# Optimization experiments

Measured on AMD Instinct MI355X. Metric: run time of the kernel, lower is better.

Reference implementation:

```python
import jax, jax.numpy as jnp
import numpy as np

ROI_POOLING_SIZE = 7
CROP = ROI_POOLING_SIZE * 2  # before_pooling_size = 14


def _crop_and_resize(img, boxes, crop):
    """tf.image.crop_and_resize (bilinear, extrapolation_value=0) for a single image.

    img:   [H, W, C]
    boxes: [N, 4] normalized [y1, x1, y2, x2]
    returns [N, crop, crop, C]
    """
    H, W, C = img.shape
    y1, x1, y2, x2 = boxes[:, 0], boxes[:, 1], boxes[:, 2], boxes[:, 3]
    idx = jnp.arange(crop, dtype=img.dtype)  # crop > 1 branch of TF semantics
    # sample coordinates in source-pixel space: [N, crop]
    ys = y1[:, None] * (H - 1) + idx[None, :] * ((y2 - y1) * (H - 1) / (crop - 1))[:, None]
    xs = x1[:, None] * (W - 1) + idx[None, :] * ((x2 - x1) * (W - 1) / (crop - 1))[:, None]

    y0f = jnp.floor(ys)
    x0f = jnp.floor(xs)
    ly = ys - y0f  # bilinear fractional weights [N, crop]
    lx = xs - x0f

    y0 = jnp.clip(y0f.astype(jnp.int32), 0, H - 1)
    y1i = jnp.clip(y0 + 1, 0, H - 1)
    x0 = jnp.clip(x0f.astype(jnp.int32), 0, W - 1)
    x1i = jnp.clip(x0 + 1, 0, W - 1)

    # out-of-image samples get extrapolation_value = 0
    vy = (ys >= 0) & (ys <= H - 1)  # [N, crop]
    vx = (xs >= 0) & (xs <= W - 1)

    # irregular per-box bilinear gather: val[n,i,j,c] = img[y[n,i], x[n,j], c]
    def g(yi, xi):
        return img[yi[:, :, None], xi[:, None, :]]  # [N, crop, crop, C]

    v00 = g(y0, x0)
    v01 = g(y0, x1i)
    v10 = g(y1i, x0)
    v11 = g(y1i, x1i)

    lxb = lx[:, None, :, None]
    lyb = ly[:, :, None, None]
    top = v00 + (v01 - v00) * lxb
    bot = v10 + (v11 - v10) * lxb
    val = top + (bot - top) * lyb

    valid = (vy[:, :, None] & vx[:, None, :])[..., None]
    return jnp.where(valid, val, jnp.zeros((), dtype=img.dtype))


def reference(feature_maps, proposals, image_shape):
    # proposals are pixel-space [x1, y1, x2, y2]; normalize to [y1/h, x1/w, y2/h, x2/w]
    h = image_shape[0].astype(jnp.float32)
    w = image_shape[1].astype(jnp.float32)
    boxes = jnp.stack(
        [proposals[:, 1] / h, proposals[:, 0] / w, proposals[:, 3] / h, proposals[:, 2] / w],
        axis=1,
    )
    crops = _crop_and_resize(feature_maps[0], boxes, CROP)  # [N, 14, 14, C]
    N, Hc, Wc, C = crops.shape
    # MaxPooling2D(pool=2, stride=2, padding='same'); 14 is even so no padding needed
    pooled = crops.reshape(N, Hc // 2, 2, Wc // 2, 2, C).max(axis=(2, 4))
    return pooled  # [N, 7, 7, C]


def setup_inputs() -> dict:
    key = jax.random.key(0)
    k1, k2, k3, k4, k5 = jax.random.split(key, 5)
    H_img, W_img = 800, 1216
    N = 2000
    feature_maps = jax.random.normal(k1, (1, 200, 304, 256), dtype=jnp.float32)
    # realistic boxes in image pixel coords [x1, y1, x2, y2]
    x1 = jax.random.uniform(k2, (N,), minval=0.0, maxval=0.75 * W_img)
    y1 = jax.random.uniform(k3, (N,), minval=0.0, maxval=0.75 * H_img)
    bw = jax.random.uniform(k4, (N,), minval=16.0, maxval=0.25 * W_img)
    bh = jax.random.uniform(k5, (N,), minval=16.0, maxval=0.25 * H_img)
    proposals = jnp.stack([x1, y1, jnp.minimum(x1 + bw, W_img - 1.0), jnp.minimum(y1 + bh, H_img - 1.0)], axis=1).astype(jnp.float32)
    image_shape = jnp.array([H_img, W_img], dtype=jnp.int32)
    return {"feature_maps": feature_maps, "proposals": proposals, "image_shape": image_shape}
```

## Files before the change

### kernel.cpp

```cpp
#include <hip/hip_runtime.h>
#include <math.h>

#define H_FM 200
#define W_FM 304
#define C_FM 256
#define NPIX (H_FM * W_FM)
#define CROP 14
#define PH 7
#define NPOS 49
#define NSAMP (NPOS * 4)
#define SLABS 16
#define SLAB_C 16
#define SLAB_ELEMS (NPIX * SLAB_C)
#define SPIXB (SLAB_C * 4)
#define PIXB (C_FM * 4)

typedef float floatx4 __attribute__((ext_vector_type(4)));

#define TP 16
__global__ __launch_bounds__(256) void repack_kernel(
    const float* __restrict__ fm,
    float*       __restrict__ slabbed)
{
    __shared__ float lds[TP][C_FM + 4];
    const int tid = threadIdx.x;
    const int p0  = blockIdx.x * TP;

    const float4* src = (const float4*)(fm + (size_t)p0 * C_FM);
    #pragma unroll
    for (int i = 0; i < 4; ++i) {
        const int idx = i * 256 + tid;
        const float4 v = src[idx];
        const int pix = idx >> 6;
        const int c4  = idx & 63;
        *(float4*)&lds[pix][c4 * 4] = v;
    }
    __syncthreads();

    const int s = tid >> 4;
    const int j = tid & 15;
    float* dst = slabbed + (size_t)s * SLAB_ELEMS + (size_t)p0 * SLAB_C;
    #pragma unroll
    for (int k = 0; k < 4; ++k) {
        const int m   = k * 16 + j;
        const int pix = m >> 2;
        const int cq  = m & 3;
        const float4 v = *(const float4*)&lds[pix][s * SLAB_C + cq * 4];
        *(float4*)(dst + m * 4) = v;
    }
}

__global__ __launch_bounds__(256) void roi_pool_slab_kernel(
    const float* __restrict__ slabbed,
    const float* __restrict__ proposals,
    const int*   __restrict__ image_shape,
    float*       __restrict__ out,
    int N)
{
    __shared__ uint2  gOD[224];
    __shared__ float4 gW[224];

    const int bid   = blockIdx.x;
    const int xcd   = bid & 7;
    const int jj    = bid >> 3;
    const int phase = jj / N;
    const int n     = jj - phase * N;
    const int slab  = phase * 8 + xcd;

    const int tid = threadIdx.x;

    if (tid < NSAMP) {
        const int s  = tid & 3;
        const int p  = tid >> 2;
        const int py = p / PH;
        const int px = p - py * PH;
        const int a  = s >> 1;
        const int b  = s & 1;

        const float himg = (float)image_shape[0];
        const float wimg = (float)image_shape[1];

        const float bx1 = proposals[n * 4 + 0] / wimg;
        const float by1 = proposals[n * 4 + 1] / himg;
        const float bx2 = proposals[n * 4 + 2] / wimg;
        const float by2 = proposals[n * 4 + 3] / himg;

        const float Hm1 = (float)(H_FM - 1);
        const float Wm1 = (float)(W_FM - 1);

        const float ystep = (by2 - by1) * Hm1 / (float)(CROP - 1);
        const float xstep = (bx2 - bx1) * Wm1 / (float)(CROP - 1);
        const float ys = by1 * Hm1 + (float)(2 * py + a) * ystep;
        const float xs = bx1 * Wm1 + (float)(2 * px + b) * xstep;

        const float y0f = floorf(ys);
        const float x0f = floorf(xs);
        const float ly  = ys - y0f;
        const float lx  = xs - x0f;

        int y0 = min(max((int)y0f, 0), H_FM - 1);
        int x0 = min(max((int)x0f, 0), W_FM - 1);
        const int dy = min(y0 + 1, H_FM - 1) - y0;
        const int dx = min(x0 + 1, W_FM - 1) - x0;

        const bool valid = (ys >= 0.0f) && (ys <= Hm1) &&
                           (xs >= 0.0f) && (xs <= Wm1);
        const float vf   = valid ? 1.0f : 0.0f;
        const float omlx = 1.0f - lx;
        const float omly = 1.0f - ly;

        float4 w;
        w.x = omlx * omly * vf;
        w.y = lx   * omly * vf;
        w.z = omlx * ly   * vf;
        w.w = lx   * ly   * vf;

        uint2 od;
        od.x = (uint32_t)(y0 * W_FM + x0) * SPIXB;
        od.y = (uint32_t)(dx * SPIXB) | ((uint32_t)(dy * W_FM * SPIXB) << 16);

        const int esk = tid + (tid >> 3);
        gOD[esk] = od;
        gW[esk]  = w;
    }
    __syncthreads();

    const int wave = tid >> 6;
    const int lane = tid & 63;
    const int p    = wave * 16 + (lane >> 2);
    const int q    = lane & 3;
    const int pa   = min(p, NPOS - 1);

    const char* base = (const char*)slabbed + (size_t)slab * (SLAB_ELEMS * sizeof(float));
    const uint32_t qB = (uint32_t)q * 16u;

    float4 m;
    #pragma unroll
    for (int s = 0; s < 4; ++s) {
        const int e   = pa * 4 + s;
        const int esk = e + (e >> 3);
        const uint2  od = gOD[esk];
        const float4 w  = gW[esk];

        const uint32_t o00 = od.x + qB;
        const uint32_t dxB = od.y & 0xffffu;
        const uint32_t dyB = od.y >> 16;

        const float4 t00 = *(const float4*)(base + o00);
        const float4 t01 = *(const float4*)(base + o00 + dxB);
        const float4 t10 = *(const float4*)(base + o00 + dyB);
        const float4 t11 = *(const float4*)(base + o00 + dxB + dyB);

        float4 v;
        v.x = fmaf(t00.x, w.x, fmaf(t01.x, w.y, fmaf(t10.x, w.z, t11.x * w.w)));
        v.y = fmaf(t00.y, w.x, fmaf(t01.y, w.y, fmaf(t10.y, w.z, t11.y * w.w)));
        v.z = fmaf(t00.z, w.x, fmaf(t01.z, w.y, fmaf(t10.z, w.z, t11.z * w.w)));
        v.w = fmaf(t00.w, w.x, fmaf(t01.w, w.y, fmaf(t10.w, w.z, t11.w * w.w)));

        if (s == 0) {
            m = v;
        } else {
            m.x = fmaxf(m.x, v.x);
            m.y = fmaxf(m.y, v.y);
            m.z = fmaxf(m.z, v.z);
            m.w = fmaxf(m.w, v.w);
        }
    }

    if (p < NPOS) {
        floatx4 mv;
        mv.x = m.x; mv.y = m.y; mv.z = m.z; mv.w = m.w;
        __builtin_nontemporal_store(mv,
            (floatx4*)(out + ((size_t)n * NPOS + p) * C_FM + slab * SLAB_C + q * 4));
    }
}

__global__ __launch_bounds__(256) void roi_pool_direct_kernel(
    const float* __restrict__ fm,
    const float* __restrict__ proposals,
    const int*   __restrict__ image_shape,
    float*       __restrict__ out,
    int N)
{
    __shared__ uint4  gO[NSAMP];
    __shared__ float4 gWf[NSAMP];

    const int n   = blockIdx.x;
    const int tid = threadIdx.x;

    if (tid < NSAMP) {
        const int s  = tid & 3;
        const int p  = tid >> 2;
        const int py = p / PH;
        const int px = p - py * PH;
        const int a  = s >> 1;
        const int b  = s & 1;

        const float himg = (float)image_shape[0];
        const float wimg = (float)image_shape[1];
        const float bx1 = proposals[n * 4 + 0] / wimg;
        const float by1 = proposals[n * 4 + 1] / himg;
        const float bx2 = proposals[n * 4 + 2] / wimg;
        const float by2 = proposals[n * 4 + 3] / himg;

        const float Hm1 = (float)(H_FM - 1);
        const float Wm1 = (float)(W_FM - 1);
        const float ystep = (by2 - by1) * Hm1 / (float)(CROP - 1);
        const float xstep = (bx2 - bx1) * Wm1 / (float)(CROP - 1);
        const float ys = by1 * Hm1 + (float)(2 * py + a) * ystep;
        const float xs = bx1 * Wm1 + (float)(2 * px + b) * xstep;

        const float y0f = floorf(ys);
        const float x0f = floorf(xs);
        const float ly  = ys - y0f;
        const float lx  = xs - x0f;
        int y0 = min(max((int)y0f, 0), H_FM - 1);
        int x0 = min(max((int)x0f, 0), W_FM - 1);
        const int dy = min(y0 + 1, H_FM - 1) - y0;
        const int dx = min(x0 + 1, W_FM - 1) - x0;
        const bool valid = (ys >= 0.0f) && (ys <= Hm1) &&
                           (xs >= 0.0f) && (xs <= Wm1);
        const float vf   = valid ? 1.0f : 0.0f;
        const float omlx = 1.0f - lx;
        const float omly = 1.0f - ly;

        float4 w;
        w.x = omlx * omly * vf;
        w.y = lx   * omly * vf;
        w.z = omlx * ly   * vf;
        w.w = lx   * ly   * vf;

        uint4 o;
        o.x = (uint32_t)(y0 * W_FM + x0) * PIXB;
        o.y = (uint32_t)dx * PIXB;
        o.z = (uint32_t)(dy * W_FM) * PIXB;
        o.w = 0u;
        gO[tid]  = o;
        gWf[tid] = w;
    }
    __syncthreads();

    const int wave = tid >> 6;
    const int lane = tid & 63;
    const uint32_t laneB = (uint32_t)lane * 16u;
    const char* fmB  = (const char*)fm;
    char*       outB = (char*)out + (size_t)n * (NPOS * PIXB);

    const int pbeg = (wave * NPOS) >> 2;
    const int pend = ((wave + 1) * NPOS) >> 2;

    for (int p = pbeg; p < pend; ++p) {
        float4 m;
        #pragma unroll
        for (int s = 0; s < 4; ++s) {
            const uint4  o = gO[p * 4 + s];
            const float4 w = gWf[p * 4 + s];
            const uint32_t o00 = o.x + laneB;
            const float4 t00 = *(const float4*)(fmB + o00);
            const float4 t01 = *(const float4*)(fmB + o00 + o.y);
            const float4 t10 = *(const float4*)(fmB + o00 + o.z);
            const float4 t11 = *(const float4*)(fmB + o00 + o.y + o.z);
            float4 v;
            v.x = fmaf(t00.x, w.x, fmaf(t01.x, w.y, fmaf(t10.x, w.z, t11.x * w.w)));
            v.y = fmaf(t00.y, w.x, fmaf(t01.y, w.y, fmaf(t10.y, w.z, t11.y * w.w)));
            v.z = fmaf(t00.z, w.x, fmaf(t01.z, w.y, fmaf(t10.z, w.z, t11.z * w.w)));
            v.w = fmaf(t00.w, w.x, fmaf(t01.w, w.y, fmaf(t10.w, w.z, t11.w * w.w)));
            if (s == 0) { m = v; }
            else {
                m.x = fmaxf(m.x, v.x); m.y = fmaxf(m.y, v.y);
                m.z = fmaxf(m.z, v.z); m.w = fmaxf(m.w, v.w);
            }
        }
        floatx4 mv;
        mv.x = m.x; mv.y = m.y; mv.z = m.z; mv.w = m.w;
        __builtin_nontemporal_store(mv,
            (floatx4*)(outB + (uint32_t)p * PIXB + laneB));
    }
}

extern "C" void kernel_launch(void* const* d_in, const int* in_sizes, int n_in,
                              void* d_out, int out_size, void* d_ws, size_t ws_size,
                              hipStream_t stream) {
    (void)n_in; (void)out_size;

    const float* fm        = (const float*)d_in[0];
    const float* proposals = (const float*)d_in[1];
    const int*   imshape   = (const int*)d_in[2];
    float* out = (float*)d_out;

    const int N = in_sizes[1] / 4;
    const size_t needed = (size_t)SLABS * SLAB_ELEMS * sizeof(float);

    if (ws_size >= needed) {
        repack_kernel<<<NPIX / TP, 256, 0, stream>>>(fm, (float*)d_ws);
        roi_pool_slab_kernel<<<SLABS * N, 256, 0, stream>>>(
            (const float*)d_ws, proposals, imshape, out, N);
    } else {
        roi_pool_direct_kernel<<<N, 256, 0, stream>>>(
            fm, proposals, imshape, out, N);
    }
}
```

Before: 215.5 us.

## Precompute ROI sample geometry in separate kernel and batch gathers in pool kernel

Adds a geom_kernel that computes per-sample offsets and bilinear weights for all ROIs into workspace tables once. Previously every slab block recomputed them, 16 times per ROI. The pool kernel now reads these tables directly, with no LDS staging or __syncthreads, and issues all 16 gathers before doing the FMAs to raise memory-level parallelism. The cost is an extra kernel launch, additional workspace (about 9.4 MB of tables), more global reads per block and higher register pressure. The new path runs only when the workspace is large enough.

```diff
diff --git a/kernel.cpp b/kernel.cpp
--- a/kernel.cpp
+++ b/kernel.cpp
@@ -15,7 +15,74 @@
 #define SPIXB (SLAB_C * 4)
 #define PIXB (C_FM * 4)
 
+#define SLAB_BYTES ((size_t)SLABS * SLAB_ELEMS * sizeof(float))
+
 typedef float floatx4 __attribute__((ext_vector_type(4)));
+
+__global__ __launch_bounds__(256) void geom_kernel(
+    const float* __restrict__ proposals,
+    const int*   __restrict__ image_shape,
+    uint2*       __restrict__ odTab,
+    float4*      __restrict__ wTab,
+    int N)
+{
+    const int g = blockIdx.x * 256 + threadIdx.x;
+    if (g >= N * NSAMP) return;
+
+    const int n = g / NSAMP;
+    const int t = g - n * NSAMP;
+    const int s  = t & 3;
+    const int p  = t >> 2;
+    const int py = p / PH;
+    const int px = p - py * PH;
+    const int a  = s >> 1;
+    const int b  = s & 1;
+
+    const float himg = (float)image_shape[0];
+    const float wimg = (float)image_shape[1];
+
+    const float bx1 = proposals[n * 4 + 0] / wimg;
+    const float by1 = proposals[n * 4 + 1] / himg;
+    const float bx2 = proposals[n * 4 + 2] / wimg;
+    const float by2 = proposals[n * 4 + 3] / himg;
+
+    const float Hm1 = (float)(H_FM - 1);
+    const float Wm1 = (float)(W_FM - 1);
+
+    const float ystep = (by2 - by1) * Hm1 / (float)(CROP - 1);
+    const float xstep = (bx2 - bx1) * Wm1 / (float)(CROP - 1);
+    const float ys = by1 * Hm1 + (float)(2 * py + a) * ystep;
+    const float xs = bx1 * Wm1 + (float)(2 * px + b) * xstep;
+
+    const float y0f = floorf(ys);
+    const float x0f = floorf(xs);
+    const float ly  = ys - y0f;
+    const float lx  = xs - x0f;
+
+    int y0 = min(max((int)y0f, 0), H_FM - 1);
+    int x0 = min(max((int)x0f, 0), W_FM - 1);
+    const int dy = min(y0 + 1, H_FM - 1) - y0;
+    const int dx = min(x0 + 1, W_FM - 1) - x0;
+
+    const bool valid = (ys >= 0.0f) && (ys <= Hm1) &&
+                       (xs >= 0.0f) && (xs <= Wm1);
+    const float vf   = valid ? 1.0f : 0.0f;
+    const float omlx = 1.0f - lx;
+    const float omly = 1.0f - ly;
+
+    float4 w;
+    w.x = omlx * omly * vf;
+    w.y = lx   * omly * vf;
+    w.z = omlx * ly   * vf;
+    w.w = lx   * ly   * vf;
+
+    uint2 od;
+    od.x = (uint32_t)(y0 * W_FM + x0) * SPIXB;
+    od.y = (uint32_t)(dx * SPIXB) | ((uint32_t)(dy * W_FM * SPIXB) << 16);
+
+    odTab[g] = od;
+    wTab[g]  = w;
+}
 
 #define TP 16
 __global__ __launch_bounds__(256) void repack_kernel(
@@ -47,6 +114,71 @@
         const int cq  = m & 3;
         const float4 v = *(const float4*)&lds[pix][s * SLAB_C + cq * 4];
         *(float4*)(dst + m * 4) = v;
+    }
+}
+
+__global__ __launch_bounds__(256) void roi_pool_tab_kernel(
+    const float* __restrict__ slabbed,
+    const uint2* __restrict__ odTab,
+    const float4* __restrict__ wTab,
+    float*       __restrict__ out,
+    int N)
+{
+    const int bid   = blockIdx.x;
+    const int xcd   = bid & 7;
+    const int jj    = bid >> 3;
+    const int phase = jj / N;
+    const int n     = jj - phase * N;
+    const int slab  = phase * 8 + xcd;
+
+    const int tid  = threadIdx.x;
+    const int wave = tid >> 6;
+    const int lane = tid & 63;
+    const int p    = wave * 16 + (lane >> 2);
+    const int q    = lane & 3;
+    const int pa   = min(p, NPOS - 1);
+
+    const char* base = (const char*)slabbed + (size_t)slab * SLAB_BYTES / SLABS;
+    const uint32_t qB = (uint32_t)q * 16u;
+    const int tbase = n * NSAMP + pa * 4;
+
+    uint2  od[4];
+    float4 wv[4];
+    #pragma unroll
+    for (int s = 0; s < 4; ++s) {
+        od[s] = odTab[tbase + s];
+        wv[s] = wTab[tbase + s];
+    }
+
+    float4 t00[4], t01[4], t10[4], t11[4];
+    #pragma unroll
+    for (int s = 0; s < 4; ++s) {
+        const uint32_t o00 = od[s].x + qB;
+        const uint32_t dxB = od[s].y & 0xffffu;
+        const uint32_t dyB = od[s].y >> 16;
+        t00[s] = *(const float4*)(base + o00);
+        t01[s] = *(const float4*)(base + o00 + dxB);
+        t10[s] = *(const float4*)(base + o00 + dyB);
+        t11[s] = *(const float4*)(base + o00 + dxB + dyB);
+    }
+
+    float4 v[4];
+    #pragma unroll
+    for (int s = 0; s < 4; ++s) {
+        v[s].x = fmaf(t00[s].x, wv[s].x, fmaf(t01[s].x, wv[s].y, fmaf(t10[s].x, wv[s].z, t11[s].x * wv[s].w)));
+        v[s].y = fmaf(t00[s].y, wv[s].x, fmaf(t01[s].y, wv[s].y, fmaf(t10[s].y, wv[s].z, t11[s].y * wv[s].w)));
+        v[s].z = fmaf(t00[s].z, wv[s].x, fmaf(t01[s].z, wv[s].y, fmaf(t10[s].z, wv[s].z, t11[s].z * wv[s].w)));
+        v[s].w = fmaf(t00[s].w, wv[s].x, fmaf(t01[s].w, wv[s].y, fmaf(t10[s].w, wv[s].z, t11[s].w * wv[s].w)));
+    }
+
+    if (p < NPOS) {
+        floatx4 m;
+        m.x = fmaxf(fmaxf(v[0].x, v[1].x), fmaxf(v[2].x, v[3].x));
+        m.y = fmaxf(fmaxf(v[0].y, v[1].y), fmaxf(v[2].y, v[3].y));
+        m.z = fmaxf(fmaxf(v[0].z, v[1].z), fmaxf(v[2].z, v[3].z));
+        m.w = fmaxf(fmaxf(v[0].w, v[1].w), fmaxf(v[2].w, v[3].w));
+        __builtin_nontemporal_store(m,
+            (floatx4*)(out + ((size_t)n * NPOS + p) * C_FM + slab * SLAB_C + q * 4));
     }
 }
 
@@ -79,7 +211,6 @@
 
         const float himg = (float)image_shape[0];
         const float wimg = (float)image_shape[1];
-
         const float bx1 = proposals[n * 4 + 0] / wimg;
         const float by1 = proposals[n * 4 + 1] / himg;
         const float bx2 = proposals[n * 4 + 2] / wimg;
@@ -87,7 +218,6 @@
 
         const float Hm1 = (float)(H_FM - 1);
         const float Wm1 = (float)(W_FM - 1);
-
         const float ystep = (by2 - by1) * Hm1 / (float)(CROP - 1);
         const float xstep = (bx2 - bx1) * Wm1 / (float)(CROP - 1);
         const float ys = by1 * Hm1 + (float)(2 * py + a) * ystep;
@@ -97,12 +227,10 @@
         const float x0f = floorf(xs);
         const float ly  = ys - y0f;
         const float lx  = xs - x0f;
-
         int y0 = min(max((int)y0f, 0), H_FM - 1);
         int x0 = min(max((int)x0f, 0), W_FM - 1);
         const int dy = min(y0 + 1, H_FM - 1) - y0;
         const int dx = min(x0 + 1, W_FM - 1) - x0;
-
         const bool valid = (ys >= 0.0f) && (ys <= Hm1) &&
                            (xs >= 0.0f) && (xs <= Wm1);
         const float vf   = valid ? 1.0f : 0.0f;
@@ -141,29 +269,22 @@
         const int esk = e + (e >> 3);
         const uint2  od = gOD[esk];
         const float4 w  = gW[esk];
-
         const uint32_t o00 = od.x + qB;
         const uint32_t dxB = od.y & 0xffffu;
         const uint32_t dyB = od.y >> 16;
-
         const float4 t00 = *(const float4*)(base + o00);
         const float4 t01 = *(const float4*)(base + o00 + dxB);
         const float4 t10 = *(const float4*)(base + o00 + dyB);
         const float4 t11 = *(const float4*)(base + o00 + dxB + dyB);
-
         float4 v;
         v.x = fmaf(t00.x, w.x, fmaf(t01.x, w.y, fmaf(t10.x, w.z, t11.x * w.w)));
         v.y = fmaf(t00.y, w.x, fmaf(t01.y, w.y, fmaf(t10.y, w.z, t11.y * w.w)));
         v.z = fmaf(t00.z, w.x, fmaf(t01.z, w.y, fmaf(t10.z, w.z, t11.z * w.w)));
         v.w = fmaf(t00.w, w.x, fmaf(t01.w, w.y, fmaf(t10.w, w.z, t11.w * w.w)));
-
-        if (s == 0) {
-            m = v;
-        } else {
-            m.x = fmaxf(m.x, v.x);
-            m.y = fmaxf(m.y, v.y);
-            m.z = fmaxf(m.z, v.z);
-            m.w = fmaxf(m.w, v.w);
+        if (s == 0) { m = v; }
+        else {
+            m.x = fmaxf(m.x, v.x); m.y = fmaxf(m.y, v.y);
+            m.z = fmaxf(m.z, v.z); m.w = fmaxf(m.w, v.w);
         }
     }
 
@@ -289,9 +410,22 @@
     float* out = (float*)d_out;
 
     const int N = in_sizes[1] / 4;
-    const size_t needed = (size_t)SLABS * SLAB_ELEMS * sizeof(float);
-
-    if (ws_size >= needed) {
+    const int nsamp_total = N * NSAMP;
+
+    const size_t od_bytes   = (size_t)nsamp_total * sizeof(uint2);
+    const size_t w_bytes    = (size_t)nsamp_total * sizeof(float4);
+    const size_t need_slab  = SLAB_BYTES;
+    const size_t need_full  = need_slab + od_bytes + w_bytes;
+
+    if (ws_size >= need_full) {
+        uint2*  odTab = (uint2*)((char*)d_ws + need_slab);
+        float4* wTab  = (float4*)((char*)d_ws + need_slab + od_bytes);
+        geom_kernel<<<(nsamp_total + 255) / 256, 256, 0, stream>>>(
+            proposals, imshape, odTab, wTab, N);
+        repack_kernel<<<NPIX / TP, 256, 0, stream>>>(fm, (float*)d_ws);
+        roi_pool_tab_kernel<<<SLABS * N, 256, 0, stream>>>(
+            (const float*)d_ws, odTab, wTab, out, N);
+    } else if (ws_size >= need_slab) {
         repack_kernel<<<NPIX / TP, 256, 0, stream>>>(fm, (float*)d_ws);
         roi_pool_slab_kernel<<<SLABS * N, 256, 0, stream>>>(
             (const float*)d_ws, proposals, imshape, out, N);
```

Result: slower. 260.5 us (+20.9%).

## Precompute separable per-ROI row/column bilinear geometry in a separate kernel

Applied to the files above, without the earlier changes.

Adds a geom_kernel that computes, for each ROI, 14 row and 14 column sample descriptors (offset, two weights, neighbour stride) into a workspace table, using the separability of bilinear weights. A new pooling kernel reads four descriptors per thread and forms the four corner weights as products, removing the per-block LDS setup and __syncthreads. Each of the 16 slab blocks per ROI previously recomputed the same 196-sample geometry. The trade-off is an extra kernel launch and a small global table read per block.

```diff
diff --git a/kernel.cpp b/kernel.cpp
--- a/kernel.cpp
+++ b/kernel.cpp
@@ -14,8 +14,67 @@
 #define SLAB_ELEMS (NPIX * SLAB_C)
 #define SPIXB (SLAB_C * 4)
 #define PIXB (C_FM * 4)
+#define GEOM_PER_ROI 28
+
+#define SLAB_BYTES ((size_t)SLABS * SLAB_ELEMS * sizeof(float))
 
 typedef float floatx4 __attribute__((ext_vector_type(4)));
+
+__global__ __launch_bounds__(256) void geom_kernel(
+    const float* __restrict__ proposals,
+    const int*   __restrict__ image_shape,
+    uint4*       __restrict__ geomTab,
+    int N)
+{
+    const int g = blockIdx.x * 256 + threadIdx.x;
+    if (g >= N * GEOM_PER_ROI) return;
+
+    const int n = g / GEOM_PER_ROI;
+    const int e = g - n * GEOM_PER_ROI;
+
+    const float himg = (float)image_shape[0];
+    const float wimg = (float)image_shape[1];
+
+    const float bx1 = proposals[n * 4 + 0] / wimg;
+    const float by1 = proposals[n * 4 + 1] / himg;
+    const float bx2 = proposals[n * 4 + 2] / wimg;
+    const float by2 = proposals[n * 4 + 3] / himg;
+
+    const float Hm1 = (float)(H_FM - 1);
+    const float Wm1 = (float)(W_FM - 1);
+
+    uint4 out;
+    if (e < CROP) {
+        const int i = e;
+        const float ystep = (by2 - by1) * Hm1 / (float)(CROP - 1);
+        const float ys    = by1 * Hm1 + (float)i * ystep;
+        const float y0f   = floorf(ys);
+        const float ly    = ys - y0f;
+        int y0 = min(max((int)y0f, 0), H_FM - 1);
+        const int dy = min(y0 + 1, H_FM - 1) - y0;
+        const bool vy = (ys >= 0.0f) && (ys <= Hm1);
+        const float vf = vy ? 1.0f : 0.0f;
+        out.x = (uint32_t)(y0 * W_FM) * SPIXB;
+        out.y = __float_as_uint((1.0f - ly) * vf);
+        out.z = __float_as_uint(ly * vf);
+        out.w = (uint32_t)(dy * W_FM) * SPIXB;
+    } else {
+        const int j = e - CROP;
+        const float xstep = (bx2 - bx1) * Wm1 / (float)(CROP - 1);
+        const float xs    = bx1 * Wm1 + (float)j * xstep;
+        const float x0f   = floorf(xs);
+        const float lx    = xs - x0f;
+        int x0 = min(max((int)x0f, 0), W_FM - 1);
+        const int dx = min(x0 + 1, W_FM - 1) - x0;
+        const bool vx = (xs >= 0.0f) && (xs <= Wm1);
+        const float vf = vx ? 1.0f : 0.0f;
+        out.x = (uint32_t)x0 * SPIXB;
+        out.y = __float_as_uint((1.0f - lx) * vf);
+        out.z = __float_as_uint(lx * vf);
+        out.w = (uint32_t)dx * SPIXB;
+    }
+    geomTab[g] = out;
+}
 
 #define TP 16
 __global__ __launch_bounds__(256) void repack_kernel(
@@ -50,6 +109,83 @@
     }
 }
 
+__global__ __launch_bounds__(256) void roi_pool_fac_kernel(
+    const float* __restrict__ slabbed,
+    const uint4* __restrict__ geomTab,
+    float*       __restrict__ out,
+    int N)
+{
+    const int bid   = blockIdx.x;
+    const int xcd   = bid & 7;
+    const int jj    = bid >> 3;
+    const int phase = jj / N;
+    const int n     = jj - phase * N;
+    const int slab  = phase * 8 + xcd;
+
+    const int tid  = threadIdx.x;
+    const int wave = tid >> 6;
+    const int lane = tid & 63;
+    const int p    = wave * 16 + (lane >> 2);
+    const int q    = lane & 3;
+    const int pa   = min(p, NPOS - 1);
+    const int py   = pa / PH;
+    const int px   = pa - py * PH;
+
+    const char* base = (const char*)slabbed + (size_t)slab * (SLAB_ELEMS * sizeof(float));
+    const uint32_t qB = (uint32_t)q * 16u;
+
+    const uint4* gt = geomTab + n * GEOM_PER_ROI;
+    const uint4 yg0 = gt[2 * py];
+    const uint4 yg1 = gt[2 * py + 1];
+    const uint4 xg0 = gt[CROP + 2 * px];
+    const uint4 xg1 = gt[CROP + 2 * px + 1];
+
+    float4 m;
+    #pragma unroll
+    for (int s = 0; s < 4; ++s) {
+        const uint4 yg = (s & 2) ? yg1 : yg0;
+        const uint4 xg = (s & 1) ? xg1 : xg0;
+
+        const uint32_t o00 = yg.x + xg.x + qB;
+        const uint32_t dxB = xg.w;
+        const uint32_t dyB = yg.w;
+
+        const float wt = __uint_as_float(yg.y);
+        const float wb = __uint_as_float(yg.z);
+        const float wl = __uint_as_float(xg.y);
+        const float wr = __uint_as_float(xg.z);
+
+        const float w00 = wt * wl;
+        const float w01 = wt * wr;
+        const float w10 = wb * wl;
+        const float w11 = wb * wr;
+
+        const float4 t00 = *(const float4*)(base + o00);
+        const float4 t01 = *(const float4*)(base + o00 + dxB);
+        const float4 t10 = *(const float4*)(base + o00 + dyB);
+        const float4 t11 = *(const float4*)(base + o00 + dxB + dyB);
+
+        float4 v;
+        v.x = fmaf(t00.x, w00, fmaf(t01.x, w01, fmaf(t10.x, w10, t11.x * w11)));
+        v.y = fmaf(t00.y, w00, fmaf(t01.y, w01, fmaf(t10.y, w10, t11.y * w11)));
+        v.z = fmaf(t00.z, w00, fmaf(t01.z, w01, fmaf(t10.z, w10, t11.z * w11)));
+        v.w = fmaf(t00.w, w00, fmaf(t01.w, w01, fmaf(t10.w, w10, t11.w * w11)));
+
+        if (s == 0) { m = v; }
+        else {
+            m.x = fmaxf(m.x, v.x); m.y = fmaxf(m.y, v.y);
+            m.z = fmaxf(m.z, v.z); m.w = fmaxf(m.w, v.w);
+        }
+    }
+
+    if (p < NPOS) {
+        floatx4 mv;
+        mv.x = m.x; mv.y = m.y; mv.z = m.z; mv.w = m.w;
+        __builtin_nontemporal_store(mv,
+            (floatx4*)(out + ((size_t)n * NPOS + p) * C_FM + slab * SLAB_C + q * 4));
+    }
+}
+
 __global__ __launch_bounds__(256) void roi_pool_slab_kernel(
     const float* __restrict__ slabbed,
     const float* __restrict__ proposals,
@@ -79,7 +215,6 @@
 
         const float himg = (float)image_shape[0];
         const float wimg = (float)image_shape[1];
-
         const float bx1 = proposals[n * 4 + 0] / wimg;
         const float by1 = proposals[n * 4 + 1] / himg;
         const float bx2 = proposals[n * 4 + 2] / wimg;
@@ -87,7 +222,6 @@
 
         const float Hm1 = (float)(H_FM - 1);
         const float Wm1 = (float)(W_FM - 1);
-
         const float ystep = (by2 - by1) * Hm1 / (float)(CROP - 1);
         const float xstep = (bx2 - bx1) * Wm1 / (float)(CROP - 1);
         const float ys = by1 * Hm1 + (float)(2 * py + a) * ystep;
@@ -97,12 +231,10 @@
         const float x0f = floorf(xs);
         const float ly  = ys - y0f;
         const float lx  = xs - x0f;
-
         int y0 = min(max((int)y0f, 0), H_FM - 1);
         int x0 = min(max((int)x0f, 0), W_FM - 1);
         const int dy = min(y0 + 1, H_FM - 1) - y0;
         const int dx = min(x0 + 1, W_FM - 1) - x0;
-
         const bool valid = (ys >= 0.0f) && (ys <= Hm1) &&
                            (xs >= 0.0f) && (xs <= Wm1);
         const float vf   = valid ? 1.0f : 0.0f;
@@ -141,29 +273,22 @@
         const int esk = e + (e >> 3);
         const uint2  od = gOD[esk];
         const float4 w  = gW[esk];
-
         const uint32_t o00 = od.x + qB;
         const uint32_t dxB = od.y & 0xffffu;
         const uint32_t dyB = od.y >> 16;
-
         const float4 t00 = *(const float4*)(base + o00);
         const float4 t01 = *(const float4*)(base + o00 + dxB);
         const float4 t10 = *(const float4*)(base + o00 + dyB);
         const float4 t11 = *(const float4*)(base + o00 + dxB + dyB);
-
         float4 v;
         v.x = fmaf(t00.x, w.x, fmaf(t01.x, w.y, fmaf(t10.x, w.z, t11.x * w.w)));
         v.y = fmaf(t00.y, w.x, fmaf(t01.y, w.y, fmaf(t10.y, w.z, t11.y * w.w)));
         v.z = fmaf(t00.z, w.x, fmaf(t01.z, w.y, fmaf(t10.z, w.z, t11.z * w.w)));
         v.w = fmaf(t00.w, w.x, fmaf(t01.w, w.y, fmaf(t10.w, w.z, t11.w * w.w)));
-
-        if (s == 0) {
-            m = v;
-        } else {
-            m.x = fmaxf(m.x, v.x);
-            m.y = fmaxf(m.y, v.y);
-            m.z = fmaxf(m.z, v.z);
-            m.w = fmaxf(m.w, v.w);
+        if (s == 0) { m = v; }
+        else {
+            m.x = fmaxf(m.x, v.x); m.y = fmaxf(m.y, v.y);
+            m.z = fmaxf(m.z, v.z); m.w = fmaxf(m.w, v.w);
         }
     }
 
@@ -289,9 +414,20 @@
     float* out = (float*)d_out;
 
     const int N = in_sizes[1] / 4;
-    const size_t needed = (size_t)SLABS * SLAB_ELEMS * sizeof(float);
-
-    if (ws_size >= needed) {
+    const int ngeom = N * GEOM_PER_ROI;
+
+    const size_t geom_bytes = (size_t)ngeom * sizeof(uint4);
+    const size_t need_slab  = SLAB_BYTES;
+    const size_t need_full  = need_slab + geom_bytes;
+
+    if (ws_size >= need_full) {
+        uint4* geomTab = (uint4*)((char*)d_ws + need_slab);
+        geom_kernel<<<(ngeom + 255) / 256, 256, 0, stream>>>(
+            proposals, imshape, geomTab, N);
+        repack_kernel<<<NPIX / TP, 256, 0, stream>>>(fm, (float*)d_ws);
+        roi_pool_fac_kernel<<<SLABS * N, 256, 0, stream>>>(
+            (const float*)d_ws, geomTab, out, N);
+    } else if (ws_size >= need_slab) {
         repack_kernel<<<NPIX / TP, 256, 0, stream>>>(fm, (float*)d_ws);
         roi_pool_slab_kernel<<<SLABS * N, 256, 0, stream>>>(
             (const float*)d_ws, proposals, imshape, out, N);
```

Result: slower. 246.4 us (+14.3%).
